# Optimization experiments

Hardware: AMD Instinct MI355X
Metric: run time of the kernel (lower is better)

## Reference

```python
import jax, jax.numpy as jnp
import numpy as np

N_NODES = 50000
N_EDGES = 800000
D_IN = 64
H1 = 64
H2 = 64
N_CLASSES = 10
N_GRAPHS = 500


def setup_inputs() -> dict:
    key = jax.random.key(0)
    ks = jax.random.split(key, 9)
    x = jax.random.normal(ks[0], (N_NODES, D_IN), dtype=jnp.float32)
    edge_index = jax.random.randint(ks[1], (2, N_EDGES), 0, N_NODES, dtype=jnp.int64)
    batch = jnp.sort(jax.random.randint(ks[2], (N_NODES,), 0, N_GRAPHS, dtype=jnp.int64))
    # Linear params (Kaiming-uniform-ish scale)
    def lin(k, fin, fout):
        kw, kb = jax.random.split(k)
        s = 1.0 / np.sqrt(fin)
        W = jax.random.uniform(kw, (fin, fout), minval=-s, maxval=s, dtype=jnp.float32)
        b = jax.random.uniform(kb, (fout,), minval=-s, maxval=s, dtype=jnp.float32)
        return W, b
    W1, b1 = lin(ks[3], D_IN, H1)
    W2, b2 = lin(ks[4], H1, H2)
    W3, b3 = lin(ks[5], H2, N_CLASSES)
    return {"x": x, "edge_index": edge_index, "batch": batch,
            "W1": W1, "b1": b1, "W2": W2, "b2": b2, "W3": W3, "b3": b3}


def _gin_conv(h, src, dst, W, b, eps=0.0):
    # sum aggregation of neighbor messages: msg[i] = sum_{(j->i)} h[j]
    agg = jax.ops.segment_sum(h[src], dst, num_segments=N_NODES)
    return ((1.0 + eps) * h + agg) @ W + b


def reference(x, edge_index, batch, W1, b1, W2, b2, W3, b3):
    src, dst = edge_index[0], edge_index[1]
    h = jax.nn.relu(_gin_conv(x, src, dst, W1, b1))
    h = jax.nn.relu(_gin_conv(h, src, dst, W2, b2))
    # global mean pool over graphs
    sums = jax.ops.segment_sum(h, batch, num_segments=N_GRAPHS)
    cnt = jax.ops.segment_sum(jnp.ones((N_NODES,), dtype=h.dtype), batch, num_segments=N_GRAPHS)
    pooled = sums / jnp.maximum(cnt, 1.0)[:, None]
    return pooled @ W3 + b3
```

## Files before the change

### kernel.cpp

```cpp
#include <hip/hip_runtime.h>
#include <hip/hip_bf16.h>
#include <hip/hip_fp16.h>


#define N_FEAT 64
#define CHUNK 2048
#define CAP 6144

typedef _Float16 f16;
typedef _Float16 half8 __attribute__((ext_vector_type(8)));
typedef float float4v __attribute__((ext_vector_type(4)));

__device__ inline f16 cvt_f16(float v) { return (f16)v; }
__device__ inline f16 cvt_f16(f16 v) { return v; }

template <typename TIN>
__global__ void gemm_mfma(const TIN* __restrict__ X, const float* __restrict__ W,
                          f16* __restrict__ Z, int nrows) {
    __shared__ f16 sX[64][72];
    __shared__ f16 sWT[64][72];
    int t = threadIdx.x;
    int base = blockIdx.x * 64;
    for (int idx = t; idx < 4096; idx += 256) {
        int k = idx >> 6, n = idx & 63;
        sWT[n][k] = (f16)W[idx];
    }
    for (int idx = t; idx < 4096; idx += 256) {
        int r = idx >> 6, c = idx & 63;
        int row = base + r;
        sX[r][c] = (row < nrows) ? cvt_f16(X[(size_t)row * 64 + c]) : (f16)0.f;
    }
    __syncthreads();
    int wave = t >> 6;
    int lane = t & 63;
    int quad = lane >> 4;
    int m16 = lane & 15;
    half8 a0 = *(const half8*)&sX[wave * 16 + m16][quad * 8];
    half8 a1 = *(const half8*)&sX[wave * 16 + m16][32 + quad * 8];
    float4v acc[4];
#pragma unroll
    for (int C = 0; C < 4; ++C) {
        half8 b0 = *(const half8*)&sWT[C * 16 + m16][quad * 8];
        half8 b1 = *(const half8*)&sWT[C * 16 + m16][32 + quad * 8];
        float4v d = {0.f, 0.f, 0.f, 0.f};
        d = __builtin_amdgcn_mfma_f32_16x16x32_f16(a0, b0, d, 0, 0, 0);
        d = __builtin_amdgcn_mfma_f32_16x16x32_f16(a1, b1, d, 0, 0, 0);
        acc[C] = d;
    }
#pragma unroll
    for (int reg = 0; reg < 4; ++reg) {
        int row = base + wave * 16 + quad * 4 + reg;
        if (row < nrows) {
#pragma unroll
            for (int C = 0; C < 4; ++C)
                Z[(size_t)row * 64 + C * 16 + m16] = (f16)acc[C][reg];
        }
    }
}

__global__ void bucket_scatter(const int* __restrict__ src, const int* __restrict__ dst,
                               int* __restrict__ ccur, int2* __restrict__ staging, int E) {
    __shared__ int esrc[CHUNK];
    __shared__ int edst[CHUNK];
    __shared__ int hist[256];
    __shared__ int base[256];
    int t = threadIdx.x;
    int begin = blockIdx.x * CHUNK;
    int cnt = min(CHUNK, E - begin);
    hist[t] = 0;
    __syncthreads();
    for (int i = t; i < cnt; i += 256) {
        int d = dst[begin + i];
        esrc[i] = src[begin + i];
        edst[i] = d;
        atomicAdd(&hist[d >> 8], 1);
    }
    __syncthreads();
    int h = hist[t];
    if (h > 0) base[t] = atomicAdd(&ccur[t], h);
    hist[t] = 0;
    __syncthreads();
    for (int i = t; i < cnt; i += 256) {
        int d = edst[i];
        int b = d >> 8;
        int off = base[b] + atomicAdd(&hist[b], 1);
        if (off < CAP) staging[(size_t)b * CAP + off] = make_int2(esrc[i], d);
    }
}

__global__ void bucket_finalize(const int2* __restrict__ staging, const int* __restrict__ ccur,
                                int2* __restrict__ rowse, int* __restrict__ col, int N) {
    __shared__ int2 edges[CAP];
    __shared__ int hist[256];
    __shared__ int scan[256];
    __shared__ int cur[256];
    int b = blockIdx.x, t = threadIdx.x;
    int cnt = min(ccur[b], CAP);
    int sbase = b * CAP;
    hist[t] = 0;
    __syncthreads();
    for (int i = t; i < cnt; i += 256) {
        int2 e = staging[(size_t)sbase + i];
        edges[i] = e;
        atomicAdd(&hist[e.y & 255], 1);
    }
    __syncthreads();
    int v = hist[t];
    scan[t] = v;
    __syncthreads();
    for (int off = 1; off < 256; off <<= 1) {
        int u = (t >= off) ? scan[t - off] : 0;
        __syncthreads();
        scan[t] += u;
        __syncthreads();
    }
    int excl = scan[t] - v;
    cur[t] = excl;
    int node = b * 256 + t;
    if (node < N) rowse[node] = make_int2(sbase + excl, sbase + excl + v);
    __syncthreads();
    for (int i = t; i < cnt; i += 256) {
        int2 e = edges[i];
        int pos = sbase + atomicAdd(&cur[e.y & 255], 1);
        col[pos] = e.x;
    }
}

__global__ void gather_relu(const f16* __restrict__ Z, const int2* __restrict__ rowse,
                            const int* __restrict__ col, const float* __restrict__ bias,
                            f16* __restrict__ H, int n) {
    int node = (int)((blockIdx.x * blockDim.x + threadIdx.x) >> 6);
    if (node >= n) return;
    int lane = threadIdx.x & 63;
    int g = lane >> 4, l = lane & 15;
    int2 se = rowse[node];
    int lo = se.x, hi = se.y;
    const float2* Z2 = reinterpret_cast<const float2*>(Z);
    float ax = 0.f, ay = 0.f, az = 0.f, aw = 0.f;
    int j = lo + g;
    while (j + 12 < hi) {
        int s0 = col[j], s1 = col[j + 4], s2 = col[j + 8], s3 = col[j + 12];
        float2 r0 = Z2[(size_t)s0 * 16 + l];
        float2 r1 = Z2[(size_t)s1 * 16 + l];
        float2 r2 = Z2[(size_t)s2 * 16 + l];
        float2 r3 = Z2[(size_t)s3 * 16 + l];
        float2 f;
        f = __half22float2(*(__half2*)&r0.x); ax += f.x; ay += f.y;
        f = __half22float2(*(__half2*)&r0.y); az += f.x; aw += f.y;
        f = __half22float2(*(__half2*)&r1.x); ax += f.x; ay += f.y;
        f = __half22float2(*(__half2*)&r1.y); az += f.x; aw += f.y;
        f = __half22float2(*(__half2*)&r2.x); ax += f.x; ay += f.y;
        f = __half22float2(*(__half2*)&r2.y); az += f.x; aw += f.y;
        f = __half22float2(*(__half2*)&r3.x); ax += f.x; ay += f.y;
        f = __half22float2(*(__half2*)&r3.y); az += f.x; aw += f.y;
        j += 16;
    }
    for (; j < hi; j += 4) {
        float2 r = Z2[(size_t)col[j] * 16 + l];
        float2 f0 = __half22float2(*(__half2*)&r.x);
        float2 f1 = __half22float2(*(__half2*)&r.y);
        ax += f0.x; ay += f0.y; az += f1.x; aw += f1.y;
    }
    ax += __shfl_xor(ax, 16); ay += __shfl_xor(ay, 16);
    az += __shfl_xor(az, 16); aw += __shfl_xor(aw, 16);
    ax += __shfl_xor(ax, 32); ay += __shfl_xor(ay, 32);
    az += __shfl_xor(az, 32); aw += __shfl_xor(aw, 32);
    if (g == 0) {
        float2 sr = Z2[(size_t)node * 16 + l];
        float2 fs0 = __half22float2(*(__half2*)&sr.x);
        float2 fs1 = __half22float2(*(__half2*)&sr.y);
        float4 b = reinterpret_cast<const float4*>(bias)[l];
        __half2 o0 = __floats2half2_rn(fmaxf(fs0.x + ax + b.x, 0.f),
                                       fmaxf(fs0.y + ay + b.y, 0.f));
        __half2 o1 = __floats2half2_rn(fmaxf(fs1.x + az + b.z, 0.f),
                                       fmaxf(fs1.y + aw + b.w, 0.f));
        float2 outv;
        *(__half2*)&outv.x = o0;
        *(__half2*)&outv.y = o1;
        reinterpret_cast<float2*>(H)[(size_t)node * 16 + l] = outv;
    }
}

__global__ void pool_head(const f16* __restrict__ H, const int* __restrict__ batch,
                          const float* __restrict__ W3, const float* __restrict__ b3,
                          float* __restrict__ out, int n, int ncls) {
    int gidx = blockIdx.x;
    __shared__ int bounds[2];
    __shared__ float sred[4 * 64];
    __shared__ float row[64];
    int t = threadIdx.x;
    int w = t >> 6;
    int lane = t & 63;
    int g = lane >> 4, l = lane & 15;
    if (t < 2) {
        int target = gidx + t;
        int lo = 0, hi = n;
        while (lo < hi) { int m = (lo + hi) >> 1; if (batch[m] < target) lo = m + 1; else hi = m; }
        bounds[t] = lo;
    }
    __syncthreads();
    int lo = bounds[0], hi = bounds[1];
    const float2* H2 = reinterpret_cast<const float2*>(H);
    float ax = 0.f, ay = 0.f, az = 0.f, aw = 0.f;
    for (int i = lo + (w * 4 + g); i < hi; i += 16) {
        float2 raw = H2[(size_t)i * 16 + l];
        float2 f0 = __half22float2(*(__half2*)&raw.x);
        float2 f1 = __half22float2(*(__half2*)&raw.y);
        ax += f0.x; ay += f0.y; az += f1.x; aw += f1.y;
    }
    ax += __shfl_xor(ax, 16); ay += __shfl_xor(ay, 16);
    az += __shfl_xor(az, 16); aw += __shfl_xor(aw, 16);
    ax += __shfl_xor(ax, 32); ay += __shfl_xor(ay, 32);
    az += __shfl_xor(az, 32); aw += __shfl_xor(aw, 32);
    if (g == 0) {
        sred[w * 64 + l * 4 + 0] = ax;
        sred[w * 64 + l * 4 + 1] = ay;
        sred[w * 64 + l * 4 + 2] = az;
        sred[w * 64 + l * 4 + 3] = aw;
    }
    __syncthreads();
    if (w == 0) {
        float s = sred[lane] + sred[64 + lane] + sred[128 + lane] + sred[192 + lane];
        row[lane] = s / fmaxf((float)(hi - lo), 1.0f);
    }
    __syncthreads();
    if (t < ncls) {
        float o = b3[t];
#pragma unroll
        for (int k = 0; k < 64; ++k) o += row[k] * W3[k * ncls + t];
        out[gidx * ncls + t] = o;
    }
}

extern "C" void kernel_launch(void* const* d_in, const int* in_sizes, int n_in,
                              void* d_out, int out_size, void* d_ws, size_t ws_size,
                              hipStream_t stream) {
    const float* x     = (const float*)d_in[0];
    const int*   ei    = (const int*)d_in[1];
    const int*   batch = (const int*)d_in[2];
    const float* W1    = (const float*)d_in[3];
    const float* b1    = (const float*)d_in[4];
    const float* W2    = (const float*)d_in[5];
    const float* b2    = (const float*)d_in[6];
    const float* W3    = (const float*)d_in[7];
    const float* b3    = (const float*)d_in[8];
    float* out = (float*)d_out;

    const int N = in_sizes[0] / N_FEAT;
    const int E = in_sizes[1] / 2;
    const int NCLS = 10;
    const int G = out_size / NCLS;
    const int* src = ei;
    const int* dst = ei + E;
    const int nb = (N + 255) / 256;

    int2* staging = (int2*)d_ws;
    int2* rowse   = staging + (size_t)nb * CAP;
    int*  col     = (int*)(rowse + N);
    int*  ccur    = col + (size_t)nb * CAP;
    f16*  zbuf    = (f16*)(ccur + 256);
    f16*  hbuf    = zbuf + (size_t)N * 64;

    const int gemmGrid = (N + 63) / 64;
    const int gatherGrid = (N + 3) / 4;
    const int scatGrid = (E + CHUNK - 1) / CHUNK;

    hipMemsetAsync(ccur, 0, 256 * sizeof(int), stream);
    bucket_scatter<<<scatGrid, 256, 0, stream>>>(src, dst, ccur, staging, E);
    bucket_finalize<<<nb, 256, 0, stream>>>(staging, ccur, rowse, col, N);

    gemm_mfma<float><<<gemmGrid, 256, 0, stream>>>(x, W1, zbuf, N);
    gather_relu<<<gatherGrid, 256, 0, stream>>>(zbuf, rowse, col, b1, hbuf, N);

    gemm_mfma<f16><<<gemmGrid, 256, 0, stream>>>(hbuf, W2, zbuf, N);
    gather_relu<<<gatherGrid, 256, 0, stream>>>(zbuf, rowse, col, b2, hbuf, N);

    pool_head<<<G, 256, 0, stream>>>(hbuf, batch, W3, b3, out, N, NCLS);
}
```

Baseline: 190.8 us.

## Pack staged edges to 32-bit and split gather features across two blocks

Bucket staging now stores each edge as a single int: the low 16 bits hold the source and the next 8 bits hold the low byte of the destination. This halves staging traffic and the shared-memory footprint in both bucketing kernels. The scatter chunk size is doubled. The gather kernel now uses two blocks per group of nodes, each covering half of the feature columns with 8 edge groups of 8 lanes, which raises parallelism but reads the column indices twice. Source packing assumes node ids fit in 16 bits.

After: 211.2 us. 1.11x slower.

```diff
diff --git a/kernel.cpp b/kernel.cpp
--- a/kernel.cpp
+++ b/kernel.cpp
@@ -4,7 +4,7 @@
 
 
 #define N_FEAT 64
-#define CHUNK 2048
+#define CHUNK 4096
 #define CAP 6144
 
 typedef _Float16 f16;
@@ -59,9 +59,9 @@
 }
 
 __global__ void bucket_scatter(const int* __restrict__ src, const int* __restrict__ dst,
-                               int* __restrict__ ccur, int2* __restrict__ staging, int E) {
-    __shared__ int esrc[CHUNK];
-    __shared__ int edst[CHUNK];
+                               int* __restrict__ ccur, int* __restrict__ staging, int E) {
+    __shared__ int epack[CHUNK];
+    __shared__ int ebkt[CHUNK];
     __shared__ int hist[256];
     __shared__ int base[256];
     int t = threadIdx.x;
@@ -71,8 +71,9 @@
     __syncthreads();
     for (int i = t; i < cnt; i += 256) {
         int d = dst[begin + i];
-        esrc[i] = src[begin + i];
-        edst[i] = d;
+        int s = src[begin + i];
+        epack[i] = (s & 0xFFFF) | ((d & 255) << 16);
+        ebkt[i] = d >> 8;
         atomicAdd(&hist[d >> 8], 1);
     }
     __syncthreads();
@@ -81,16 +82,15 @@
     hist[t] = 0;
     __syncthreads();
     for (int i = t; i < cnt; i += 256) {
-        int d = edst[i];
-        int b = d >> 8;
+        int b = ebkt[i];
         int off = base[b] + atomicAdd(&hist[b], 1);
-        if (off < CAP) staging[(size_t)b * CAP + off] = make_int2(esrc[i], d);
-    }
-}
-
-__global__ void bucket_finalize(const int2* __restrict__ staging, const int* __restrict__ ccur,
+        if (off < CAP) staging[(size_t)b * CAP + off] = epack[i];
+    }
+}
+
+__global__ void bucket_finalize(const int* __restrict__ staging, const int* __restrict__ ccur,
                                 int2* __restrict__ rowse, int* __restrict__ col, int N) {
-    __shared__ int2 edges[CAP];
+    __shared__ int edges[CAP];
     __shared__ int hist[256];
     __shared__ int scan[256];
     __shared__ int cur[256];
@@ -100,9 +100,9 @@
     hist[t] = 0;
     __syncthreads();
     for (int i = t; i < cnt; i += 256) {
-        int2 e = staging[(size_t)sbase + i];
+        int e = staging[(size_t)sbase + i];
         edges[i] = e;
-        atomicAdd(&hist[e.y & 255], 1);
+        atomicAdd(&hist[(e >> 16) & 255], 1);
     }
     __syncthreads();
     int v = hist[t];
@@ -120,56 +120,56 @@
     if (node < N) rowse[node] = make_int2(sbase + excl, sbase + excl + v);
     __syncthreads();
     for (int i = t; i < cnt; i += 256) {
-        int2 e = edges[i];
-        int pos = sbase + atomicAdd(&cur[e.y & 255], 1);
-        col[pos] = e.x;
+        int e = edges[i];
+        int pos = sbase + atomicAdd(&cur[(e >> 16) & 255], 1);
+        col[pos] = e & 0xFFFF;
     }
 }
 
 __global__ void gather_relu(const f16* __restrict__ Z, const int2* __restrict__ rowse,
                             const int* __restrict__ col, const float* __restrict__ bias,
                             f16* __restrict__ H, int n) {
-    int node = (int)((blockIdx.x * blockDim.x + threadIdx.x) >> 6);
+    int wave = threadIdx.x >> 6;
+    int node = (blockIdx.x >> 1) * 4 + wave;
     if (node >= n) return;
+    int half = blockIdx.x & 1;
     int lane = threadIdx.x & 63;
-    int g = lane >> 4, l = lane & 15;
+    int g = lane >> 3;
+    int l = lane & 7;
+    int rb = half * 8 + l;
     int2 se = rowse[node];
     int lo = se.x, hi = se.y;
     const float2* Z2 = reinterpret_cast<const float2*>(Z);
     float ax = 0.f, ay = 0.f, az = 0.f, aw = 0.f;
     int j = lo + g;
-    while (j + 12 < hi) {
-        int s0 = col[j], s1 = col[j + 4], s2 = col[j + 8], s3 = col[j + 12];
-        float2 r0 = Z2[(size_t)s0 * 16 + l];
-        float2 r1 = Z2[(size_t)s1 * 16 + l];
-        float2 r2 = Z2[(size_t)s2 * 16 + l];
-        float2 r3 = Z2[(size_t)s3 * 16 + l];
+    while (j + 8 < hi) {
+        int s0 = col[j], s1 = col[j + 8];
+        float2 r0 = Z2[(size_t)s0 * 16 + rb];
+        float2 r1 = Z2[(size_t)s1 * 16 + rb];
         float2 f;
         f = __half22float2(*(__half2*)&r0.x); ax += f.x; ay += f.y;
         f = __half22float2(*(__half2*)&r0.y); az += f.x; aw += f.y;
         f = __half22float2(*(__half2*)&r1.x); ax += f.x; ay += f.y;
         f = __half22float2(*(__half2*)&r1.y); az += f.x; aw += f.y;
-        f = __half22float2(*(__half2*)&r2.x); ax += f.x; ay += f.y;
-        f = __half22float2(*(__half2*)&r2.y); az += f.x; aw += f.y;
-        f = __half22float2(*(__half2*)&r3.x); ax += f.x; ay += f.y;
-        f = __half22float2(*(__half2*)&r3.y); az += f.x; aw += f.y;
         j += 16;
     }
-    for (; j < hi; j += 4) {
-        float2 r = Z2[(size_t)col[j] * 16 + l];
+    for (; j < hi; j += 8) {
+        float2 r = Z2[(size_t)col[j] * 16 + rb];
         float2 f0 = __half22float2(*(__half2*)&r.x);
         float2 f1 = __half22float2(*(__half2*)&r.y);
         ax += f0.x; ay += f0.y; az += f1.x; aw += f1.y;
     }
+    ax += __shfl_xor(ax, 8);  ay += __shfl_xor(ay, 8);
+    az += __shfl_xor(az, 8);  aw += __shfl_xor(aw, 8);
     ax += __shfl_xor(ax, 16); ay += __shfl_xor(ay, 16);
     az += __shfl_xor(az, 16); aw += __shfl_xor(aw, 16);
     ax += __shfl_xor(ax, 32); ay += __shfl_xor(ay, 32);
     az += __shfl_xor(az, 32); aw += __shfl_xor(aw, 32);
     if (g == 0) {
-        float2 sr = Z2[(size_t)node * 16 + l];
+        float2 sr = Z2[(size_t)node * 16 + rb];
         float2 fs0 = __half22float2(*(__half2*)&sr.x);
         float2 fs1 = __half22float2(*(__half2*)&sr.y);
-        float4 b = reinterpret_cast<const float4*>(bias)[l];
+        float4 b = reinterpret_cast<const float4*>(bias)[rb];
         __half2 o0 = __floats2half2_rn(fmaxf(fs0.x + ax + b.x, 0.f),
                                        fmaxf(fs0.y + ay + b.y, 0.f));
         __half2 o1 = __floats2half2_rn(fmaxf(fs1.x + az + b.z, 0.f),
@@ -177,7 +177,7 @@
         float2 outv;
         *(__half2*)&outv.x = o0;
         *(__half2*)&outv.y = o1;
-        reinterpret_cast<float2*>(H)[(size_t)node * 16 + l] = outv;
+        reinterpret_cast<float2*>(H)[(size_t)node * 16 + rb] = outv;
     }
 }
 
@@ -254,15 +254,15 @@
     const int* dst = ei + E;
     const int nb = (N + 255) / 256;
 
-    int2* staging = (int2*)d_ws;
-    int2* rowse   = staging + (size_t)nb * CAP;
+    int*  staging = (int*)d_ws;
+    int2* rowse   = (int2*)(staging + (size_t)nb * CAP);
     int*  col     = (int*)(rowse + N);
     int*  ccur    = col + (size_t)nb * CAP;
     f16*  zbuf    = (f16*)(ccur + 256);
     f16*  hbuf    = zbuf + (size_t)N * 64;
 
     const int gemmGrid = (N + 63) / 64;
-    const int gatherGrid = (N + 3) / 4;
+    const int gatherGrid = 2 * ((N + 3) / 4);
     const int scatGrid = (E + CHUNK - 1) / CHUNK;
 
     hipMemsetAsync(ccur, 0, 256 * sizeof(int), stream);
```
